# Optimization experiments

Measured on AMD Instinct MI355X. Metric: run time of the kernel, lower is better.

The kernel has to match this reference:

```python
import jax, jax.numpy as jnp
import numpy as np

N_NODES = 50000
N_EDGES = 800000
N_GRAPHS = 64
IN_CH = 128
HID_G = 256
HID_FC = 256
OUT_CH = 128


def setup_inputs() -> dict:
    key = jax.random.key(0)
    ks = jax.random.split(key, 16)
    x = jax.random.normal(ks[0], (N_NODES, IN_CH), dtype=jnp.float32)
    edge_index = jax.random.randint(ks[1], (2, N_EDGES), 0, N_NODES, dtype=jnp.int64)
    batch = jnp.sort(jax.random.randint(ks[2], (N_NODES,), 0, N_GRAPHS, dtype=jnp.int64))
    hlr = jax.random.normal(ks[3], (N_GRAPHS, 1), dtype=jnp.float32)
    std = jax.random.normal(ks[4], (N_GRAPHS, 1), dtype=jnp.float32)
    s = 0.05
    W0 = jax.random.normal(ks[5], (IN_CH, HID_G), dtype=jnp.float32) * s
    b0 = jnp.zeros((HID_G,), jnp.float32)
    W1 = jax.random.normal(ks[6], (HID_G, HID_G), dtype=jnp.float32) * s
    b1 = jnp.zeros((HID_G,), jnp.float32)
    W2 = jax.random.normal(ks[7], (HID_G, HID_G), dtype=jnp.float32) * s
    b2 = jnp.zeros((HID_G,), jnp.float32)
    fcW0 = jax.random.normal(ks[8], (HID_G + 2, HID_FC), dtype=jnp.float32) * s
    fcb0 = jnp.zeros((HID_FC,), jnp.float32)
    fcW1 = jax.random.normal(ks[9], (HID_FC, OUT_CH), dtype=jnp.float32) * s
    fcb1 = jnp.zeros((OUT_CH,), jnp.float32)
    return dict(x=x, edge_index=edge_index, batch=batch, hlr=hlr, std=std,
                W0=W0, b0=b0, W1=W1, b1=b1, W2=W2, b2=b2,
                fcW0=fcW0, fcb0=fcb0, fcW1=fcW1, fcb1=fcb1)


def _gcn_conv(h, W, b, src, dst, dis):
    # GCNConv with added self-loops and symmetric normalization:
    # out_i = sum_{j->i} d_j^{-1/2} d_i^{-1/2} (h_j W) + d_i^{-1} (h_i W) + b
    hW = h @ W  # [N, F]
    norm = dis[src] * dis[dst]  # [E]
    agg = jax.ops.segment_sum(hW[src] * norm[:, None], dst, num_segments=N_NODES)
    agg = agg + hW * (dis * dis)[:, None]  # self-loop contribution
    return agg + b


def reference(x, edge_index, batch, hlr, std, W0, b0, W1, b1, W2, b2, fcW0, fcb0, fcW1, fcb1):
    src, dst = edge_index[0], edge_index[1]
    # degree on A + I (edge weight 1), computed at destination nodes
    deg = jax.ops.segment_sum(jnp.ones((N_EDGES,), x.dtype), dst, num_segments=N_NODES) + 1.0
    dis = jax.lax.rsqrt(deg)
    h = jax.nn.relu(_gcn_conv(x, W0, b0, src, dst, dis))
    h = jax.nn.relu(_gcn_conv(h, W1, b1, src, dst, dis))
    h = jax.nn.relu(_gcn_conv(h, W2, b2, src, dst, dis))
    # global mean pool over graphs
    counts = jax.ops.segment_sum(jnp.ones((N_NODES,), x.dtype), batch, num_segments=N_GRAPHS)
    pooled = jax.ops.segment_sum(h, batch, num_segments=N_GRAPHS) / jnp.maximum(counts, 1.0)[:, None]
    z = jnp.concatenate([pooled, hlr, std], axis=1)  # [G, HID_G + 2]
    z = jax.nn.relu(z @ fcW0 + fcb0)
    return z @ fcW1 + fcb1
```

## Files before the change

### kernel.cpp

```cpp
#include <hip/hip_runtime.h>

#define NNODES 50000
#define NEDGES 800000
#define NGRAPHS 64
#define INCH 128
#define HID 256
#define ZSTR (HID + 2)
#define SCAN_B 512
#define SCAN_NB ((NNODES + SCAN_B - 1) / SCAN_B)

typedef __attribute__((ext_vector_type(8))) short short8v;
typedef __attribute__((ext_vector_type(8))) unsigned short ushort8v;
typedef __attribute__((ext_vector_type(4))) float f32x4;

__device__ inline ushort f2b(float f) {
    union { float f; unsigned u; } v; v.f = f;
    unsigned r = (v.u + 0x7FFFu + ((v.u >> 16) & 1u)) >> 16;
    return (ushort)r;
}
__device__ inline float b2f(ushort b) {
    union { unsigned u; float f; } v; v.u = ((unsigned)b) << 16;
    return v.f;
}

__global__ __launch_bounds__(256) void fill_pre(const int* __restrict__ dst, int* __restrict__ deg,
                                                unsigned char* __restrict__ pwn) {
    int e = blockIdx.x * 256 + threadIdx.x;
    if (e < NEDGES) pwn[e] = (unsigned char)atomicAdd(&deg[dst[e]], 1);
}

__global__ __launch_bounds__(256) void dis_kernel(const int* __restrict__ deg, float* __restrict__ dis) {
    int i = blockIdx.x * 256 + threadIdx.x;
    if (i < NNODES) dis[i] = rsqrtf((float)deg[i] + 1.0f);
}

__global__ __launch_bounds__(SCAN_B) void scan1(const int* __restrict__ deg, int* __restrict__ row_ptr,
                                                int* __restrict__ bsum) {
    __shared__ int s[SCAN_B];
    int t = threadIdx.x;
    int i = blockIdx.x * SCAN_B + t;
    int v = (i < NNODES) ? deg[i] : 0;
    s[t] = v;
    __syncthreads();
    for (int off = 1; off < SCAN_B; off <<= 1) {
        int x = (t >= off) ? s[t - off] : 0;
        __syncthreads();
        if (t >= off) s[t] += x;
        __syncthreads();
    }
    if (i < NNODES) row_ptr[i + 1] = s[t];
    if (t == SCAN_B - 1) bsum[blockIdx.x] = s[t];
}

__global__ __launch_bounds__(128) void scan2(int* __restrict__ bsum) {
    __shared__ int s[128];
    int t = threadIdx.x;
    int v = (t < SCAN_NB) ? bsum[t] : 0;
    s[t] = v;
    __syncthreads();
    for (int off = 1; off < 128; off <<= 1) {
        int x = (t >= off) ? s[t - off] : 0;
        __syncthreads();
        if (t >= off) s[t] += x;
        __syncthreads();
    }
    if (t < SCAN_NB) bsum[t] = s[t];
}

__global__ __launch_bounds__(SCAN_B) void scan3(int* __restrict__ row_ptr, const int* __restrict__ bsum) {
    int b = blockIdx.x, t = threadIdx.x;
    int i = b * SCAN_B + t;
    if (i == 0) row_ptr[0] = 0;
    if (i < NNODES && b > 0) row_ptr[i + 1] += bsum[b - 1];
}

__global__ __launch_bounds__(256) void fill_scatter(const int* __restrict__ src, const int* __restrict__ dst,
                                                    const unsigned char* __restrict__ pwn,
                                                    const int* __restrict__ row_ptr,
                                                    ushort* __restrict__ csr_src) {
    int e = blockIdx.x * 256 + threadIdx.x;
    if (e >= NEDGES) return;
    int d = dst[e];
    csr_src[row_ptr[d] + pwn[e]] = (ushort)src[e];
}

__global__ __launch_bounds__(256) void xcvt(const float4* __restrict__ x, const float* __restrict__ dis,
                                            ushort4* __restrict__ xb, int n4) {
    int i = blockIdx.x * 256 + threadIdx.x;
    if (i >= n4) return;
    float d = dis[i >> 5];
    float4 v = x[i];
    ushort4 o;
    o.x = f2b(d * v.x); o.y = f2b(d * v.y); o.z = f2b(d * v.z); o.w = f2b(d * v.w);
    xb[i] = o;
}

__global__ __launch_bounds__(256) void wcvt(const float* __restrict__ W, ushort* __restrict__ Wt, int K, int N) {
    int i = blockIdx.x * 256 + threadIdx.x;
    if (i >= K * N) return;
    int k = i / N, n = i - k * N;
    Wt[n * K + k] = f2b(W[i]);
}

template <int K, bool POOL>
__global__ __launch_bounds__(512, 4) void gcn_fused(const ushort* __restrict__ hin,
                                                    const int* __restrict__ row_ptr,
                                                    const ushort* __restrict__ csr_src,
                                                    const ushort* __restrict__ Bt,
                                                    const float* __restrict__ bias,
                                                    const float* __restrict__ dis,
                                                    ushort* __restrict__ hout, int scale_out,
                                                    const int* __restrict__ batch, float* __restrict__ z) {
    __shared__ ushort As[128 * K];
    __shared__ float z_loc[2][HID];
    const int tid = threadIdx.x;
    const int w = tid >> 6, l = tid & 63;
    const int R0 = blockIdx.x * 128;

    if (POOL) {
        z_loc[tid >> 8][tid & 255] = 0.f;
    }

    constexpr int CHL = K / 8;
    constexpr int NPW = 64 / CHL;
    const int sub = l / CHL;
    const int lane = l - sub * CHL;
    const ushort* hp = hin + lane * 8;
#pragma unroll
    for (int it = 0; it < 128 / (8 * NPW); ++it) {
        int nloc = (it * 8 + w) * NPW + sub;
        int node = R0 + nloc;
        ushort8v o;
        if (node < NNODES) {
            ushort8v sv = *(const ushort8v*)&hp[(size_t)node * K];
            float a0 = b2f(sv[0]), a1 = b2f(sv[1]), a2 = b2f(sv[2]), a3 = b2f(sv[3]);
            float a4 = b2f(sv[4]), a5 = b2f(sv[5]), a6 = b2f(sv[6]), a7 = b2f(sv[7]);
            int e = row_ptr[node], e1 = row_ptr[node + 1];
            for (; e + 7 < e1; e += 8) {
                ushort8v v[8];
#pragma unroll
                for (int u = 0; u < 8; ++u) v[u] = *(const ushort8v*)&hp[(size_t)csr_src[e + u] * K];
#pragma unroll
                for (int u = 0; u < 8; ++u) {
                    a0 += b2f(v[u][0]); a1 += b2f(v[u][1]); a2 += b2f(v[u][2]); a3 += b2f(v[u][3]);
                    a4 += b2f(v[u][4]); a5 += b2f(v[u][5]); a6 += b2f(v[u][6]); a7 += b2f(v[u][7]);
                }
            }
            for (; e < e1; ++e) {
                ushort8v v0 = *(const ushort8v*)&hp[(size_t)csr_src[e] * K];
                a0 += b2f(v0[0]); a1 += b2f(v0[1]); a2 += b2f(v0[2]); a3 += b2f(v0[3]);
                a4 += b2f(v0[4]); a5 += b2f(v0[5]); a6 += b2f(v0[6]); a7 += b2f(v0[7]);
            }
            o[0] = f2b(a0); o[1] = f2b(a1); o[2] = f2b(a2); o[3] = f2b(a3);
            o[4] = f2b(a4); o[5] = f2b(a5); o[6] = f2b(a6); o[7] = f2b(a7);
        } else {
            o = ushort8v{0, 0, 0, 0, 0, 0, 0, 0};
        }
        *(ushort8v*)&As[nloc * K + ((lane * 8) ^ ((nloc & 7) * 8))] = o;
    }
    __syncthreads();

    const int wr = w >> 2, wc = w & 3;
    const int r16 = l & 15, kg = l >> 4;
    f32x4 acc[4][4] = {};
#pragma unroll
    for (int k0 = 0; k0 < K; k0 += 32) {
        int k = k0 + kg * 8;
        short8v a[4], b[4];
#pragma unroll
        for (int m = 0; m < 4; ++m) {
            int row = wr * 64 + m * 16 + r16;
            a[m] = *(const short8v*)&As[row * K + (k ^ ((row & 7) * 8))];
        }
#pragma unroll
        for (int n = 0; n < 4; ++n)
            b[n] = *(const short8v*)&Bt[(size_t)(wc * 64 + n * 16 + r16) * K + k];
#pragma unroll
        for (int m = 0; m < 4; ++m)
#pragma unroll
            for (int n = 0; n < 4; ++n)
                acc[m][n] = __builtin_amdgcn_mfma_f32_16x16x32_bf16(a[m], b[n], acc[m][n], 0, 0, 0);
    }
    float bv[4];
#pragma unroll
    for (int n = 0; n < 4; ++n) bv[n] = bias[wc * 64 + n * 16 + r16];

    if (!POOL) {
#pragma unroll
        for (int m = 0; m < 4; ++m) {
#pragma unroll
            for (int j = 0; j < 4; ++j) {
                int row = R0 + wr * 64 + m * 16 + kg * 4 + j;
                if (row >= NNODES) continue;
                float dr = dis[row];
                float os = scale_out ? dr : 1.0f;
#pragma unroll
                for (int n = 0; n < 4; ++n) {
                    float v = fmaxf(dr * acc[m][n][j] + bv[n], 0.f) * os;
                    hout[(size_t)row * HID + wc * 64 + n * 16 + r16] = f2b(v);
                }
            }
        }
    } else {
        const int g0 = batch[R0];
        float psum[2][4] = {{0.f, 0.f, 0.f, 0.f}, {0.f, 0.f, 0.f, 0.f}};
#pragma unroll
        for (int m = 0; m < 4; ++m) {
#pragma unroll
            for (int j = 0; j < 4; ++j) {
                int row = R0 + wr * 64 + m * 16 + kg * 4 + j;
                if (row >= NNODES) continue;
                float dr = dis[row];
                int slot = batch[row] - g0;
#pragma unroll
                for (int n = 0; n < 4; ++n) {
                    float v = fmaxf(dr * acc[m][n][j] + bv[n], 0.f);
                    if (slot <= 1) {
                        psum[slot][n] += v;
                    } else {
                        atomicAdd(&z[(size_t)(g0 + slot) * ZSTR + wc * 64 + n * 16 + r16], v);
                    }
                }
            }
        }
#pragma unroll
        for (int s = 0; s < 2; ++s)
#pragma unroll
            for (int n = 0; n < 4; ++n)
                if (psum[s][n] != 0.f) atomicAdd(&z_loc[s][wc * 64 + n * 16 + r16], psum[s][n]);
        __syncthreads();
        int last = R0 + 127;
        if (last > NNODES - 1) last = NNODES - 1;
        const int g_last = batch[last];
        const int s = tid >> 8;
        const int ch = tid & 255;
        if (g0 + s <= g_last && g0 + s < NGRAPHS) {
            float v = z_loc[s][ch];
            if (v != 0.f) atomicAdd(&z[(size_t)(g0 + s) * ZSTR + ch], v);
        }
    }
}

__global__ __launch_bounds__(256) void graph_bounds(const int* __restrict__ batch, int* __restrict__ gstart) {
    int i = blockIdx.x * 256 + threadIdx.x;
    if (i >= NNODES) return;
    int b = batch[i];
    if (i == 0) {
        for (int g = 0; g <= b; ++g) gstart[g] = 0;
    } else {
        int pb = batch[i - 1];
        for (int g = pb + 1; g <= b; ++g) gstart[g] = i;
    }
    if (i == NNODES - 1) {
        for (int g = b + 1; g <= NGRAPHS; ++g) gstart[g] = NNODES;
    }
}

__global__ __launch_bounds__(HID) void pool_finalize(const int* __restrict__ gstart, const float* __restrict__ hlr,
                                                     const float* __restrict__ stdv, float* __restrict__ z) {
    int g = blockIdx.x;
    int t = threadIdx.x;
    int cnt = gstart[g + 1] - gstart[g];
    float inv = 1.f / (float)(cnt > 0 ? cnt : 1);
    z[g * ZSTR + t] *= inv;
    if (t == 0) {
        z[g * ZSTR + HID] = hlr[g];
        z[g * ZSTR + HID + 1] = stdv[g];
    }
}

__global__ __launch_bounds__(HID) void fc_k(const float* __restrict__ z, const float* __restrict__ fcW0,
                                            const float* __restrict__ fcb0, const float* __restrict__ fcW1,
                                            const float* __restrict__ fcb1, float* __restrict__ out) {
    __shared__ float zs[ZSTR];
    __shared__ float z2[HID];
    int g = blockIdx.x;
    int t = threadIdx.x;
    zs[t] = z[g * ZSTR + t];
    if (t < 2) zs[HID + t] = z[g * ZSTR + HID + t];
    __syncthreads();
    float acc = fcb0[t];
    for (int k = 0; k < ZSTR; ++k) acc += zs[k] * fcW0[k * HID + t];
    z2[t] = fmaxf(acc, 0.f);
    __syncthreads();
    if (t < INCH) {
        float acc2 = fcb1[t];
        for (int k = 0; k < HID; ++k) acc2 += z2[k] * fcW1[k * INCH + t];
        out[g * INCH + t] = acc2;
    }
}

extern "C" void kernel_launch(void* const* d_in, const int* in_sizes, int n_in,
                              void* d_out, int out_size, void* d_ws, size_t ws_size,
                              hipStream_t stream) {
    const float* x = (const float*)d_in[0];
    const int* ei = (const int*)d_in[1];
    const int* src = ei;
    const int* dst = ei + NEDGES;
    const int* batch = (const int*)d_in[2];
    const float* hlr = (const float*)d_in[3];
    const float* stdv = (const float*)d_in[4];
    const float* W0 = (const float*)d_in[5];
    const float* b0 = (const float*)d_in[6];
    const float* W1 = (const float*)d_in[7];
    const float* b1 = (const float*)d_in[8];
    const float* W2 = (const float*)d_in[9];
    const float* b2 = (const float*)d_in[10];
    const float* fcW0 = (const float*)d_in[11];
    const float* fcb0 = (const float*)d_in[12];
    const float* fcW1 = (const float*)d_in[13];
    const float* fcb1 = (const float*)d_in[14];
    float* out = (float*)d_out;

    char* p = (char*)d_ws;
    auto alloc = [&](size_t bytes) -> char* {
        char* r = p;
        p += (bytes + 255) & ~(size_t)255;
        return r;
    };
    ushort* xb = (ushort*)alloc(sizeof(ushort) * (size_t)NNODES * INCH);
    ushort* h = (ushort*)alloc(sizeof(ushort) * (size_t)NNODES * HID);
    ushort* hb = (ushort*)alloc(sizeof(ushort) * (size_t)NNODES * HID);
    ushort* Wt0 = (ushort*)alloc(sizeof(ushort) * HID * INCH);
    ushort* Wt1 = (ushort*)alloc(sizeof(ushort) * HID * HID);
    ushort* Wt2 = (ushort*)alloc(sizeof(ushort) * HID * HID);
    float* dis = (float*)alloc(sizeof(float) * NNODES);
    int* deg = (int*)alloc(sizeof(int) * NNODES);
    int* row_ptr = (int*)alloc(sizeof(int) * (NNODES + 1));
    unsigned char* pwn = (unsigned char*)alloc(sizeof(unsigned char) * NEDGES);
    ushort* csr_src = (ushort*)alloc(sizeof(ushort) * NEDGES);
    int* bsum = (int*)alloc(sizeof(int) * 128);
    int* gstart = (int*)alloc(sizeof(int) * (NGRAPHS + 1));
    float* z = (float*)alloc(sizeof(float) * NGRAPHS * ZSTR);
    (void)ws_size; (void)in_sizes; (void)n_in; (void)out_size;

    const int eblocks = (NEDGES + 255) / 256;

    hipMemsetAsync(deg, 0, sizeof(int) * NNODES, stream);
    hipMemsetAsync(z, 0, sizeof(float) * NGRAPHS * ZSTR, stream);
    fill_pre<<<eblocks, 256, 0, stream>>>(dst, deg, pwn);
    dis_kernel<<<(NNODES + 255) / 256, 256, 0, stream>>>(deg, dis);
    scan1<<<SCAN_NB, SCAN_B, 0, stream>>>(deg, row_ptr, bsum);
    scan2<<<1, 128, 0, stream>>>(bsum);
    scan3<<<SCAN_NB, SCAN_B, 0, stream>>>(row_ptr, bsum);
    fill_scatter<<<eblocks, 256, 0, stream>>>(src, dst, pwn, row_ptr, csr_src);

    xcvt<<<(NNODES * INCH / 4 + 255) / 256, 256, 0, stream>>>((const float4*)x, dis, (ushort4*)xb,
                                                              NNODES * INCH / 4);
    wcvt<<<(INCH * HID + 255) / 256, 256, 0, stream>>>(W0, Wt0, INCH, HID);
    wcvt<<<(HID * HID + 255) / 256, 256, 0, stream>>>(W1, Wt1, HID, HID);
    wcvt<<<(HID * HID + 255) / 256, 256, 0, stream>>>(W2, Wt2, HID, HID);

    const int gblocks = (NNODES + 127) / 128;
    gcn_fused<INCH, false><<<gblocks, 512, 0, stream>>>(xb, row_ptr, csr_src, Wt0, b0, dis, h, 1, batch, z);
    gcn_fused<HID, false><<<gblocks, 512, 0, stream>>>(h, row_ptr, csr_src, Wt1, b1, dis, hb, 1, batch, z);
    gcn_fused<HID, true><<<gblocks, 512, 0, stream>>>(hb, row_ptr, csr_src, Wt2, b2, dis, h, 0, batch, z);

    graph_bounds<<<(NNODES + 255) / 256, 256, 0, stream>>>(batch, gstart);
    pool_finalize<<<NGRAPHS, HID, 0, stream>>>(gstart, hlr, stdv, z);
    fc_k<<<NGRAPHS, HID, 0, stream>>>(z, fcW0, fcb0, fcW1, fcb1, out);
}
```

Measured before the change: 319.9 us.

## Merge preprocessing kernels and fold pooling finalize into FC kernel

Folds the rsqrt degree normalization into the first scan kernel. Merges the CSR scatter, x conversion and three weight transposes into a single block-partitioned launch. Replaces graph_bounds and pool_finalize with a binary search over the sorted batch array inside the FC kernel, and adds nontemporal loads and stores on streaming edge data. This cuts about six kernel launches and their serialization gaps, at the cost of a more branchy combined kernel.

Result: slower. 328.5 us (+2.7%).

```diff
diff --git a/kernel.cpp b/kernel.cpp
--- a/kernel.cpp
+++ b/kernel.cpp
@@ -9,6 +9,11 @@
 #define SCAN_B 512
 #define SCAN_NB ((NNODES + SCAN_B - 1) / SCAN_B)
 
+#define EBLOCKS ((NEDGES + 255) / 256)
+#define XBLOCKS ((NNODES * INCH / 4 + 255) / 256)
+#define W0BLOCKS ((INCH * HID + 255) / 256)
+#define WBLOCKS ((HID * HID + 255) / 256)
+
 typedef __attribute__((ext_vector_type(8))) short short8v;
 typedef __attribute__((ext_vector_type(8))) unsigned short ushort8v;
 typedef __attribute__((ext_vector_type(4))) float f32x4;
@@ -26,20 +31,20 @@
 __global__ __launch_bounds__(256) void fill_pre(const int* __restrict__ dst, int* __restrict__ deg,
                                                 unsigned char* __restrict__ pwn) {
     int e = blockIdx.x * 256 + threadIdx.x;
-    if (e < NEDGES) pwn[e] = (unsigned char)atomicAdd(&deg[dst[e]], 1);
-}
-
-__global__ __launch_bounds__(256) void dis_kernel(const int* __restrict__ deg, float* __restrict__ dis) {
-    int i = blockIdx.x * 256 + threadIdx.x;
-    if (i < NNODES) dis[i] = rsqrtf((float)deg[i] + 1.0f);
+    if (e < NEDGES) {
+        int d = __builtin_nontemporal_load(&dst[e]);
+        unsigned char s = (unsigned char)atomicAdd(&deg[d], 1);
+        __builtin_nontemporal_store(s, &pwn[e]);
+    }
 }
 
 __global__ __launch_bounds__(SCAN_B) void scan1(const int* __restrict__ deg, int* __restrict__ row_ptr,
-                                                int* __restrict__ bsum) {
+                                                int* __restrict__ bsum, float* __restrict__ dis) {
     __shared__ int s[SCAN_B];
     int t = threadIdx.x;
     int i = blockIdx.x * SCAN_B + t;
     int v = (i < NNODES) ? deg[i] : 0;
+    if (i < NNODES) dis[i] = rsqrtf((float)v + 1.0f);
     s[t] = v;
     __syncthreads();
     for (int off = 1; off < SCAN_B; off <<= 1) {
@@ -74,32 +79,51 @@
     if (i < NNODES && b > 0) row_ptr[i + 1] += bsum[b - 1];
 }
 
-__global__ __launch_bounds__(256) void fill_scatter(const int* __restrict__ src, const int* __restrict__ dst,
-                                                    const unsigned char* __restrict__ pwn,
-                                                    const int* __restrict__ row_ptr,
-                                                    ushort* __restrict__ csr_src) {
-    int e = blockIdx.x * 256 + threadIdx.x;
-    if (e >= NEDGES) return;
-    int d = dst[e];
-    csr_src[row_ptr[d] + pwn[e]] = (ushort)src[e];
-}
-
-__global__ __launch_bounds__(256) void xcvt(const float4* __restrict__ x, const float* __restrict__ dis,
-                                            ushort4* __restrict__ xb, int n4) {
-    int i = blockIdx.x * 256 + threadIdx.x;
-    if (i >= n4) return;
-    float d = dis[i >> 5];
-    float4 v = x[i];
-    ushort4 o;
-    o.x = f2b(d * v.x); o.y = f2b(d * v.y); o.z = f2b(d * v.z); o.w = f2b(d * v.w);
-    xb[i] = o;
-}
-
-__global__ __launch_bounds__(256) void wcvt(const float* __restrict__ W, ushort* __restrict__ Wt, int K, int N) {
-    int i = blockIdx.x * 256 + threadIdx.x;
-    if (i >= K * N) return;
-    int k = i / N, n = i - k * N;
-    Wt[n * K + k] = f2b(W[i]);
+__global__ __launch_bounds__(256) void prep_all(const int* __restrict__ src, const int* __restrict__ dst,
+                                                const unsigned char* __restrict__ pwn,
+                                                const int* __restrict__ row_ptr, ushort* __restrict__ csr_src,
+                                                const float* __restrict__ x, const float* __restrict__ dis,
+                                                ushort4* __restrict__ xb,
+                                                const float* __restrict__ W0, ushort* __restrict__ Wt0,
+                                                const float* __restrict__ W1, ushort* __restrict__ Wt1,
+                                                const float* __restrict__ W2, ushort* __restrict__ Wt2) {
+    const int b = blockIdx.x;
+    const int t = threadIdx.x;
+    if (b < EBLOCKS) {
+        int e = b * 256 + t;
+        if (e < NEDGES) {
+            int d = __builtin_nontemporal_load(&dst[e]);
+            int s = __builtin_nontemporal_load(&src[e]);
+            __builtin_nontemporal_store((ushort)s, &csr_src[row_ptr[d] + pwn[e]]);
+        }
+    } else if (b < EBLOCKS + XBLOCKS) {
+        int i = (b - EBLOCKS) * 256 + t;
+        if (i < NNODES * INCH / 4) {
+            float d = dis[i >> 5];
+            f32x4 v = __builtin_nontemporal_load((const f32x4*)x + i);
+            ushort4 o;
+            o.x = f2b(d * v[0]); o.y = f2b(d * v[1]); o.z = f2b(d * v[2]); o.w = f2b(d * v[3]);
+            xb[i] = o;
+        }
+    } else if (b < EBLOCKS + XBLOCKS + W0BLOCKS) {
+        int i = (b - EBLOCKS - XBLOCKS) * 256 + t;
+        if (i < INCH * HID) {
+            int k = i / HID, n = i - k * HID;
+            Wt0[n * INCH + k] = f2b(W0[i]);
+        }
+    } else if (b < EBLOCKS + XBLOCKS + W0BLOCKS + WBLOCKS) {
+        int i = (b - EBLOCKS - XBLOCKS - W0BLOCKS) * 256 + t;
+        if (i < HID * HID) {
+            int k = i / HID, n = i - k * HID;
+            Wt1[n * HID + k] = f2b(W1[i]);
+        }
+    } else {
+        int i = (b - EBLOCKS - XBLOCKS - W0BLOCKS - WBLOCKS) * 256 + t;
+        if (i < HID * HID) {
+            int k = i / HID, n = i - k * HID;
+            Wt2[n * HID + k] = f2b(W2[i]);
+        }
+    }
 }
 
 template <int K, bool POOL>
@@ -241,43 +265,28 @@
     }
 }
 
-__global__ __launch_bounds__(256) void graph_bounds(const int* __restrict__ batch, int* __restrict__ gstart) {
-    int i = blockIdx.x * 256 + threadIdx.x;
-    if (i >= NNODES) return;
-    int b = batch[i];
-    if (i == 0) {
-        for (int g = 0; g <= b; ++g) gstart[g] = 0;
-    } else {
-        int pb = batch[i - 1];
-        for (int g = pb + 1; g <= b; ++g) gstart[g] = i;
-    }
-    if (i == NNODES - 1) {
-        for (int g = b + 1; g <= NGRAPHS; ++g) gstart[g] = NNODES;
-    }
-}
-
-__global__ __launch_bounds__(HID) void pool_finalize(const int* __restrict__ gstart, const float* __restrict__ hlr,
-                                                     const float* __restrict__ stdv, float* __restrict__ z) {
+__global__ __launch_bounds__(HID) void fc_k(const int* __restrict__ batch, const float* __restrict__ hlr,
+                                            const float* __restrict__ stdv, const float* __restrict__ z,
+                                            const float* __restrict__ fcW0, const float* __restrict__ fcb0,
+                                            const float* __restrict__ fcW1, const float* __restrict__ fcb1,
+                                            float* __restrict__ out) {
+    __shared__ float zs[ZSTR];
+    __shared__ float z2[HID];
+    __shared__ int s_cnt;
     int g = blockIdx.x;
     int t = threadIdx.x;
-    int cnt = gstart[g + 1] - gstart[g];
-    float inv = 1.f / (float)(cnt > 0 ? cnt : 1);
-    z[g * ZSTR + t] *= inv;
     if (t == 0) {
-        z[g * ZSTR + HID] = hlr[g];
-        z[g * ZSTR + HID + 1] = stdv[g];
-    }
-}
-
-__global__ __launch_bounds__(HID) void fc_k(const float* __restrict__ z, const float* __restrict__ fcW0,
-                                            const float* __restrict__ fcb0, const float* __restrict__ fcW1,
-                                            const float* __restrict__ fcb1, float* __restrict__ out) {
-    __shared__ float zs[ZSTR];
-    __shared__ float z2[HID];
-    int g = blockIdx.x;
-    int t = threadIdx.x;
-    zs[t] = z[g * ZSTR + t];
-    if (t < 2) zs[HID + t] = z[g * ZSTR + HID + t];
+        int lo = 0, hi = NNODES;
+        while (lo < hi) { int m = (lo + hi) >> 1; if (batch[m] < g) lo = m + 1; else hi = m; }
+        int a = lo;
+        lo = 0; hi = NNODES;
+        while (lo < hi) { int m = (lo + hi) >> 1; if (batch[m] < g + 1) lo = m + 1; else hi = m; }
+        s_cnt = lo - a;
+    }
+    __syncthreads();
+    float inv = 1.f / (float)(s_cnt > 0 ? s_cnt : 1);
+    zs[t] = z[g * ZSTR + t] * inv;
+    if (t < 2) zs[HID + t] = (t == 0) ? hlr[g] : stdv[g];
     __syncthreads();
     float acc = fcb0[t];
     for (int k = 0; k < ZSTR; ++k) acc += zs[k] * fcW0[k * HID + t];
@@ -330,33 +339,22 @@
     unsigned char* pwn = (unsigned char*)alloc(sizeof(unsigned char) * NEDGES);
     ushort* csr_src = (ushort*)alloc(sizeof(ushort) * NEDGES);
     int* bsum = (int*)alloc(sizeof(int) * 128);
-    int* gstart = (int*)alloc(sizeof(int) * (NGRAPHS + 1));
     float* z = (float*)alloc(sizeof(float) * NGRAPHS * ZSTR);
     (void)ws_size; (void)in_sizes; (void)n_in; (void)out_size;
 
-    const int eblocks = (NEDGES + 255) / 256;
-
     hipMemsetAsync(deg, 0, sizeof(int) * NNODES, stream);
     hipMemsetAsync(z, 0, sizeof(float) * NGRAPHS * ZSTR, stream);
-    fill_pre<<<eblocks, 256, 0, stream>>>(dst, deg, pwn);
-    dis_kernel<<<(NNODES + 255) / 256, 256, 0, stream>>>(deg, dis);
-    scan1<<<SCAN_NB, SCAN_B, 0, stream>>>(deg, row_ptr, bsum);
+    fill_pre<<<EBLOCKS, 256, 0, stream>>>(dst, deg, pwn);
+    scan1<<<SCAN_NB, SCAN_B, 0, stream>>>(deg, row_ptr, bsum, dis);
     scan2<<<1, 128, 0, stream>>>(bsum);
     scan3<<<SCAN_NB, SCAN_B, 0, stream>>>(row_ptr, bsum);
-    fill_scatter<<<eblocks, 256, 0, stream>>>(src, dst, pwn, row_ptr, csr_src);
-
-    xcvt<<<(NNODES * INCH / 4 + 255) / 256, 256, 0, stream>>>((const float4*)x, dis, (ushort4*)xb,
-                                                              NNODES * INCH / 4);
-    wcvt<<<(INCH * HID + 255) / 256, 256, 0, stream>>>(W0, Wt0, INCH, HID);
-    wcvt<<<(HID * HID + 255) / 256, 256, 0, stream>>>(W1, Wt1, HID, HID);
-    wcvt<<<(HID * HID + 255) / 256, 256, 0, stream>>>(W2, Wt2, HID, HID);
+    prep_all<<<EBLOCKS + XBLOCKS + W0BLOCKS + 2 * WBLOCKS, 256, 0, stream>>>(
+        src, dst, pwn, row_ptr, csr_src, x, dis, (ushort4*)xb, W0, Wt0, W1, Wt1, W2, Wt2);
 
     const int gblocks = (NNODES + 127) / 128;
     gcn_fused<INCH, false><<<gblocks, 512, 0, stream>>>(xb, row_ptr, csr_src, Wt0, b0, dis, h, 1, batch, z);
     gcn_fused<HID, false><<<gblocks, 512, 0, stream>>>(h, row_ptr, csr_src, Wt1, b1, dis, hb, 1, batch, z);
     gcn_fused<HID, true><<<gblocks, 512, 0, stream>>>(hb, row_ptr, csr_src, Wt2, b2, dis, h, 0, batch, z);
 
-    graph_bounds<<<(NNODES + 255) / 256, 256, 0, stream>>>(batch, gstart);
-    pool_finalize<<<NGRAPHS, HID, 0, stream>>>(gstart, hlr, stdv, z);
-    fc_k<<<NGRAPHS, HID, 0, stream>>>(z, fcW0, fcb0, fcW1, fcb1, out);
-}
+    fc_k<<<NGRAPHS, HID, 0, stream>>>(batch, hlr, stdv, z, fcW0, fcb0, fcW1, fcb1, out);
+}
```
